# Kernel tuning notes

Hardware: AMD Instinct MI355X
Metric: run time of the kernel (lower is better)

Reference implementation:

```python
import jax, jax.numpy as jnp
import numpy as np

DT = 0.001
HIDDEN = 512
OUT = 128

def setup_inputs() -> dict:
    key = jax.random.key(0)
    k1, k2 = jax.random.split(key)
    x = jax.random.normal(k1, (64, 2048, HIDDEN), dtype=jnp.float32)
    # torch Linear default init ~ U(-1/sqrt(fan_in), 1/sqrt(fan_in)), weight shape [out, in]
    lim = 1.0 / np.sqrt(HIDDEN)
    W = jax.random.uniform(k2, (OUT, HIDDEN), dtype=jnp.float32, minval=-lim, maxval=lim)
    tau_syn = jnp.asarray(0.5, dtype=jnp.float32)  # tau_syn_out (used as tau_syn_inv)
    tau_mem = jnp.asarray(0.5, dtype=jnp.float32)  # tau_mem_out (used as tau_mem_inv)
    return {"x": x, "W": W, "tau_syn": tau_syn, "tau_mem": tau_mem}

def reference(x, W, tau_syn, tau_mem):
    # SNNDecode.forward: clamp taus, permute to [seq, batch, in], per-step
    # Linear + norse LI (leaky integrator) feed-forward step with v_leak = 0.
    tau_syn = jnp.clip(tau_syn, 0.0, 1.0)
    tau_mem = jnp.clip(tau_mem, 0.0, 1.0)
    batch, seq, _ = x.shape
    # The per-step Linear is recurrence-independent: hoist it into one big GEMM.
    # z_all: [seq, batch, out]
    z_all = jnp.einsum('bsh,oh->sbo', x, W)
    v0 = jnp.zeros((batch, OUT), dtype=x.dtype)
    i0 = jnp.zeros((batch, OUT), dtype=x.dtype)

    def step(carry, z):
        v, i = carry
        # li_feed_forward_step: dv = dt*tau_mem_inv*((v_leak - v) + i)
        v_new = v + DT * tau_mem * (i - v)
        i_dec = i - DT * tau_syn * i
        i_new = i_dec + z
        return (v_new, i_new), v_new

    (v_f, i_f), voltages = jax.lax.scan(step, (v0, i0), z_all)
    # output stacked over time: [seq, batch, out]; final state (v, i)
    return voltages, v_f, i_f
```

## Files before the change

### kernel.cpp

```cpp
#include <hip/hip_runtime.h>
#include <hip/hip_bf16.h>


typedef __attribute__((ext_vector_type(4))) float f4;
typedef __attribute__((ext_vector_type(8))) short s8;

#define SEQ    2048
#define HID    512
#define CHAINS 8192
#define VOLT   16777216
#define CHUNK  64
#define NCH    32

__device__ __forceinline__ float clamp01(float x) { return fminf(fmaxf(x, 0.f), 1.f); }

__device__ __forceinline__ short f2bf(float f) {
  union { float f; unsigned u; } c; c.f = f;
  unsigned u = c.u;
  unsigned r = (u + 0x7fffu + ((u >> 16) & 1u)) >> 16;
  return (short)r;
}

__device__ __forceinline__ int swz(int row, int k) {
  return (row * 64 + k) ^ ((row & 7) << 3);
}

__global__ __launch_bounds__(256) void k_wconv(const float* __restrict__ W,
                                               unsigned short* __restrict__ Wb) {
  const int i = blockIdx.x * 256 + threadIdx.x;
  const f4 lo = ((const f4*)W)[2 * i];
  const f4 hi = ((const f4*)W)[2 * i + 1];
  s8 v;
#pragma unroll
  for (int j = 0; j < 4; ++j) { v[j] = f2bf(lo[j]); v[j + 4] = f2bf(hi[j]); }
  ((s8*)Wb)[i] = v;
}

__global__ __launch_bounds__(256, 2) void k_gemm(const float* __restrict__ X,
                                                 const unsigned short* __restrict__ Wb,
                                                 float* __restrict__ Z) {
  __shared__ short As[2][128 * 64];
  __shared__ short Bs[2][128 * 64];
  const int tid = threadIdx.x;
  const int m0  = blockIdx.x << 7;
  const int b   = m0 >> 11;
  const int t0  = m0 & 2047;

  const int rbase = tid >> 3;
  const int coff  = (tid & 7) << 3;

  const int lane = tid & 63;
  const int wid  = tid >> 6;
  const int wmb  = (wid >> 1) << 6;
  const int wnb  = (wid & 1) << 6;
  const int lr   = lane & 15;
  const int lk   = (lane >> 4) << 3;

  const float* pX[4];
  const unsigned short* pW[4];
#pragma unroll
  for (int c = 0; c < 4; ++c) {
    const int row = (c << 5) + rbase;
    pX[c] = X + (size_t)(m0 + row) * HID + coff;
    pW[c] = Wb + (size_t)row * HID + coff;
  }

  f4 acc[4][4];
#pragma unroll
  for (int mi = 0; mi < 4; ++mi)
#pragma unroll
    for (int ni = 0; ni < 4; ++ni) acc[mi][ni] = (f4){0.f, 0.f, 0.f, 0.f};

  f4 xa[2][4][2];
  s8 wv[2][4];
#pragma unroll
  for (int c = 0; c < 4; ++c) {
    xa[0][c][0] = *(const f4*)(pX[c]);
    xa[0][c][1] = *(const f4*)(pX[c] + 4);
    wv[0][c]    = *(const s8*)(pW[c]);
  }

#pragma unroll
  for (int ks = 0; ks < 8; ++ks) {
    const int cur = ks & 1;
#pragma unroll
    for (int c = 0; c < 4; ++c) {
      const int row = (c << 5) + rbase;
      s8 va;
#pragma unroll
      for (int j = 0; j < 4; ++j) {
        va[j]     = f2bf(xa[cur][c][0][j]);
        va[j + 4] = f2bf(xa[cur][c][1][j]);
      }
      *(s8*)&As[cur][swz(row, coff)] = va;
      *(s8*)&Bs[cur][swz(row, coff)] = wv[cur][c];
    }
    if (ks < 7) {
      const int k0 = (ks + 1) << 6;
#pragma unroll
      for (int c = 0; c < 4; ++c) {
        xa[cur ^ 1][c][0] = *(const f4*)(pX[c] + k0);
        xa[cur ^ 1][c][1] = *(const f4*)(pX[c] + k0 + 4);
        wv[cur ^ 1][c]    = *(const s8*)(pW[c] + k0);
      }
    }
    __syncthreads();
#pragma unroll
    for (int kk = 0; kk < 2; ++kk) {
      s8 af[4], bg[4];
#pragma unroll
      for (int mi = 0; mi < 4; ++mi)
        af[mi] = *(const s8*)&As[cur][swz(wmb + (mi << 4) + lr, (kk << 5) + lk)];
#pragma unroll
      for (int ni = 0; ni < 4; ++ni)
        bg[ni] = *(const s8*)&Bs[cur][swz(wnb + (ni << 4) + lr, (kk << 5) + lk)];
#pragma unroll
      for (int mi = 0; mi < 4; ++mi)
#pragma unroll
        for (int ni = 0; ni < 4; ++ni)
          acc[mi][ni] = __builtin_amdgcn_mfma_f32_16x16x32_bf16(af[mi], bg[ni],
                                                                acc[mi][ni], 0, 0, 0);
    }
  }

  const int rr = (lane >> 4) << 2;
#pragma unroll
  for (int mi = 0; mi < 4; ++mi) {
    const int trow = t0 + wmb + (mi << 4) + rr;
#pragma unroll
    for (int ni = 0; ni < 4; ++ni) {
      const int col = wnb + (ni << 4) + lr;
#pragma unroll
      for (int r = 0; r < 4; ++r)
        Z[(size_t)(trow + r) * 8192 + (b << 7) + col] = acc[mi][ni][r];
    }
  }
}

__global__ __launch_bounds__(256) void k_states(const float* __restrict__ tau_syn,
                                                const float* __restrict__ tau_mem,
                                                const float* __restrict__ Z,
                                                float* __restrict__ ws) {
  const int tid = threadIdx.x;
  const int cg = (blockIdx.x & 31) * 64 + (tid & 63);
  const int q  = (blockIdx.x >> 5) * 4 + (tid >> 6);
  const float a  = 0.001f * clamp01(tau_mem[0]);
  const float bb = 0.001f * clamp01(tau_syn[0]);
  const float eb = 1.f - bb;
  const f4* z4 = (const f4*)Z;
  f4 v = (f4){0.f, 0.f, 0.f, 0.f}, ii = (f4){0.f, 0.f, 0.f, 0.f};
  const int tb = q << 6;
#pragma unroll 8
  for (int j = 0; j < CHUNK; ++j) {
    f4 z = z4[(size_t)(tb + j) * 2048 + cg];
    v  = v + a * (ii - v);
    ii = eb * ii + z;
  }
  f4* vend = (f4*)ws;
  f4* iend = vend + NCH * 2048;
  vend[q * 2048 + cg] = v;
  iend[q * 2048 + cg] = ii;
}

__global__ __launch_bounds__(256) void k_combine(const float* __restrict__ tau_syn,
                                                 const float* __restrict__ tau_mem,
                                                 float* __restrict__ Out,
                                                 float* __restrict__ ws) {
  const int c = blockIdx.x * 256 + threadIdx.x;
  const float a  = 0.001f * clamp01(tau_mem[0]);
  const float bb = 0.001f * clamp01(tau_syn[0]);
  const float ea = 1.f - a, eb = 1.f - bb;
  float P = 1.f, Q = 0.f, R = 1.f;
#pragma unroll
  for (int j = 0; j < CHUNK; ++j) { float Pn = P * ea; Q = P * a + Q * eb; P = Pn; R *= eb; }
  float* vend = ws;
  float* iend = ws + NCH * CHAINS;
  float sv = 0.f, si = 0.f;
  for (int q = 0; q < NCH; ++q) {
    const int idx = q * CHAINS + c;
    const float ve = vend[idx], ie = iend[idx];
    vend[idx] = sv;  iend[idx] = si;
    const float nv = P * sv + Q * si + ve;
    si = R * si + ie;
    sv = nv;
  }
  Out[VOLT + c] = sv;
  Out[VOLT + CHAINS + c] = si;
}

__global__ __launch_bounds__(256) void k_emit(const float* __restrict__ tau_syn,
                                              const float* __restrict__ tau_mem,
                                              float* Z,
                                              const float* __restrict__ ws) {
  const int tid = threadIdx.x;
  const int cg = (blockIdx.x & 31) * 64 + (tid & 63);
  const int q  = (blockIdx.x >> 5) * 4 + (tid >> 6);
  const float a  = 0.001f * clamp01(tau_mem[0]);
  const float bb = 0.001f * clamp01(tau_syn[0]);
  const float eb = 1.f - bb;
  f4* z4 = (f4*)Z;
  const f4* vin = (const f4*)ws;
  const f4* iin = vin + NCH * 2048;
  f4 v  = vin[q * 2048 + cg];
  f4 ii = iin[q * 2048 + cg];
  const int tb = q << 6;
#pragma unroll 8
  for (int j = 0; j < CHUNK; ++j) {
    const size_t idx = (size_t)(tb + j) * 2048 + cg;
    f4 z = z4[idx];
    v  = v + a * (ii - v);
    z4[idx] = v;
    ii = eb * ii + z;
  }
}

extern "C" void kernel_launch(void* const* d_in, const int* in_sizes, int n_in,
                              void* d_out, int out_size, void* d_ws, size_t ws_size,
                              hipStream_t stream) {
  const float* X   = (const float*)d_in[0];
  const float* W   = (const float*)d_in[1];
  const float* tsy = (const float*)d_in[2];
  const float* tme = (const float*)d_in[3];
  float* Out = (float*)d_out;
  float* ws  = (float*)d_ws;
  unsigned short* Wb = (unsigned short*)((char*)d_ws + (2u << 20));

  k_wconv<<<32, 256, 0, stream>>>(W, Wb);
  k_gemm<<<1024, 256, 0, stream>>>(X, Wb, Out);
  k_states<<<256, 256, 0, stream>>>(tsy, tme, Out, ws);
  k_combine<<<32, 256, 0, stream>>>(tsy, tme, Out, ws);
  k_emit<<<256, 256, 0, stream>>>(tsy, tme, Out, ws);
}
```

Measured before the change: 128.1 us.

## Fuse chunk-state scan into GEMM epilogue via shared-memory staged output

The separate k_states kernel is removed. Each GEMM block now stages its 128x128 output tile in shared memory, writes it to Z with coalesced float4 stores, and runs the per-chunk LI recurrence over its two 64-step halves straight from LDS, writing end states to the workspace. This saves one full read of Z from global memory and a kernel launch. The bf16 packing also switches to the packed __float22bfloat162_rn conversion, and the barrier moves so the next global prefetch is issued after the LDS write sync.

```diff
diff --git a/kernel.cpp b/kernel.cpp
--- a/kernel.cpp
+++ b/kernel.cpp
@@ -2,17 +2,24 @@
 #include <hip/hip_bf16.h>
 
 
-typedef __attribute__((ext_vector_type(4))) float f4;
-typedef __attribute__((ext_vector_type(8))) short s8;
+typedef __attribute__((ext_vector_type(4))) float    f4;
+typedef __attribute__((ext_vector_type(8))) short    s8;
+typedef __attribute__((ext_vector_type(4))) unsigned u4;
 
 #define SEQ    2048
 #define HID    512
 #define CHAINS 8192
 #define VOLT   16777216
-#define CHUNK  64
 #define NCH    32
 
 __device__ __forceinline__ float clamp01(float x) { return fminf(fmaxf(x, 0.f), 1.f); }
+
+__device__ __forceinline__ unsigned pkbf(float x, float y) {
+  float2 t; t.x = x; t.y = y;
+  union { __hip_bfloat162 h; unsigned u; } c;
+  c.h = __float22bfloat162_rn(t);
+  return c.u;
+}
 
 __device__ __forceinline__ short f2bf(float f) {
   union { float f; unsigned u; } c; c.f = f;
@@ -38,13 +45,20 @@
 
 __global__ __launch_bounds__(256, 2) void k_gemm(const float* __restrict__ X,
                                                  const unsigned short* __restrict__ Wb,
-                                                 float* __restrict__ Z) {
-  __shared__ short As[2][128 * 64];
-  __shared__ short Bs[2][128 * 64];
+                                                 float* __restrict__ Z,
+                                                 const float* __restrict__ tau_syn,
+                                                 const float* __restrict__ tau_mem,
+                                                 float* __restrict__ ws) {
+  __shared__ __align__(16) char smem[65536];
+  short* const AS = (short*)smem;
+  short* const BS = (short*)(smem + 32768);
+  float* const ZS = (float*)smem;
+
   const int tid = threadIdx.x;
-  const int m0  = blockIdx.x << 7;
-  const int b   = m0 >> 11;
-  const int t0  = m0 & 2047;
+  const int blk = blockIdx.x;
+  const int m0  = blk << 7;
+  const int bI  = blk >> 4;
+  const int t0  = (blk & 15) << 7;
 
   const int rbase = tid >> 3;
   const int coff  = (tid & 7) << 3;
@@ -83,18 +97,20 @@
 #pragma unroll
   for (int ks = 0; ks < 8; ++ks) {
     const int cur = ks & 1;
+    short* const Ac = AS + (cur << 13);
+    short* const Bc = BS + (cur << 13);
 #pragma unroll
     for (int c = 0; c < 4; ++c) {
       const int row = (c << 5) + rbase;
-      s8 va;
-#pragma unroll
-      for (int j = 0; j < 4; ++j) {
-        va[j]     = f2bf(xa[cur][c][0][j]);
-        va[j + 4] = f2bf(xa[cur][c][1][j]);
-      }
-      *(s8*)&As[cur][swz(row, coff)] = va;
-      *(s8*)&Bs[cur][swz(row, coff)] = wv[cur][c];
-    }
+      u4 va;
+      va[0] = pkbf(xa[cur][c][0][0], xa[cur][c][0][1]);
+      va[1] = pkbf(xa[cur][c][0][2], xa[cur][c][0][3]);
+      va[2] = pkbf(xa[cur][c][1][0], xa[cur][c][1][1]);
+      va[3] = pkbf(xa[cur][c][1][2], xa[cur][c][1][3]);
+      *(u4*)&Ac[swz(row, coff)] = va;
+      *(s8*)&Bc[swz(row, coff)] = wv[cur][c];
+    }
+    __syncthreads();
     if (ks < 7) {
       const int k0 = (ks + 1) << 6;
 #pragma unroll
@@ -104,16 +120,15 @@
         wv[cur ^ 1][c]    = *(const s8*)(pW[c] + k0);
       }
     }
-    __syncthreads();
 #pragma unroll
     for (int kk = 0; kk < 2; ++kk) {
       s8 af[4], bg[4];
 #pragma unroll
       for (int mi = 0; mi < 4; ++mi)
-        af[mi] = *(const s8*)&As[cur][swz(wmb + (mi << 4) + lr, (kk << 5) + lk)];
+        af[mi] = *(const s8*)&Ac[swz(wmb + (mi << 4) + lr, (kk << 5) + lk)];
 #pragma unroll
       for (int ni = 0; ni < 4; ++ni)
-        bg[ni] = *(const s8*)&Bs[cur][swz(wnb + (ni << 4) + lr, (kk << 5) + lk)];
+        bg[ni] = *(const s8*)&Bc[swz(wnb + (ni << 4) + lr, (kk << 5) + lk)];
 #pragma unroll
       for (int mi = 0; mi < 4; ++mi)
 #pragma unroll
@@ -123,43 +138,44 @@
     }
   }
 
+  __syncthreads();
   const int rr = (lane >> 4) << 2;
 #pragma unroll
-  for (int mi = 0; mi < 4; ++mi) {
-    const int trow = t0 + wmb + (mi << 4) + rr;
-#pragma unroll
-    for (int ni = 0; ni < 4; ++ni) {
-      const int col = wnb + (ni << 4) + lr;
+  for (int mi = 0; mi < 4; ++mi)
+#pragma unroll
+    for (int ni = 0; ni < 4; ++ni)
 #pragma unroll
       for (int r = 0; r < 4; ++r)
-        Z[(size_t)(trow + r) * 8192 + (b << 7) + col] = acc[mi][ni][r];
-    }
-  }
-}
-
-__global__ __launch_bounds__(256) void k_states(const float* __restrict__ tau_syn,
-                                                const float* __restrict__ tau_mem,
-                                                const float* __restrict__ Z,
-                                                float* __restrict__ ws) {
-  const int tid = threadIdx.x;
-  const int cg = (blockIdx.x & 31) * 64 + (tid & 63);
-  const int q  = (blockIdx.x >> 5) * 4 + (tid >> 6);
-  const float a  = 0.001f * clamp01(tau_mem[0]);
-  const float bb = 0.001f * clamp01(tau_syn[0]);
-  const float eb = 1.f - bb;
-  const f4* z4 = (const f4*)Z;
-  f4 v = (f4){0.f, 0.f, 0.f, 0.f}, ii = (f4){0.f, 0.f, 0.f, 0.f};
-  const int tb = q << 6;
+        ZS[(wmb + (mi << 4) + rr + r) * 128 + wnb + (ni << 4) + lr] = acc[mi][ni][r];
+  __syncthreads();
+
+  {
+    float* const Zrow = Z + (size_t)t0 * 8192 + (bI << 7);
+#pragma unroll
+    for (int i = 0; i < 16; ++i) {
+      const int idx  = (i << 8) + tid;
+      const int toff = idx >> 5;
+      const int c4   = idx & 31;
+      *(f4*)(Zrow + (size_t)toff * 8192 + (c4 << 2)) = *(const f4*)&ZS[toff * 128 + (c4 << 2)];
+    }
+  }
+  {
+    const float a  = 0.001f * clamp01(tau_mem[0]);
+    const float eb = 1.f - 0.001f * clamp01(tau_syn[0]);
+    const int h = tid >> 7, col = tid & 127;
+    const float* zs = ZS + ((h << 6) * 128) + col;
+    float v = 0.f, ii = 0.f;
 #pragma unroll 8
-  for (int j = 0; j < CHUNK; ++j) {
-    f4 z = z4[(size_t)(tb + j) * 2048 + cg];
-    v  = v + a * (ii - v);
-    ii = eb * ii + z;
-  }
-  f4* vend = (f4*)ws;
-  f4* iend = vend + NCH * 2048;
-  vend[q * 2048 + cg] = v;
-  iend[q * 2048 + cg] = ii;
+    for (int j = 0; j < 64; ++j) {
+      const float z = zs[j * 128];
+      v  = v + a * (ii - v);
+      ii = eb * ii + z;
+    }
+    const int q     = ((blk & 15) << 1) + h;
+    const int chain = (bI << 7) + col;
+    ws[q * CHAINS + chain]                 = v;
+    ws[NCH * CHAINS + q * CHAINS + chain]  = ii;
+  }
 }
 
 __global__ __launch_bounds__(256) void k_combine(const float* __restrict__ tau_syn,
@@ -172,7 +188,7 @@
   const float ea = 1.f - a, eb = 1.f - bb;
   float P = 1.f, Q = 0.f, R = 1.f;
 #pragma unroll
-  for (int j = 0; j < CHUNK; ++j) { float Pn = P * ea; Q = P * a + Q * eb; P = Pn; R *= eb; }
+  for (int j = 0; j < 64; ++j) { float Pn = P * ea; Q = P * a + Q * eb; P = Pn; R *= eb; }
   float* vend = ws;
   float* iend = ws + NCH * CHAINS;
   float sv = 0.f, si = 0.f;
@@ -196,8 +212,7 @@
   const int cg = (blockIdx.x & 31) * 64 + (tid & 63);
   const int q  = (blockIdx.x >> 5) * 4 + (tid >> 6);
   const float a  = 0.001f * clamp01(tau_mem[0]);
-  const float bb = 0.001f * clamp01(tau_syn[0]);
-  const float eb = 1.f - bb;
+  const float eb = 1.f - 0.001f * clamp01(tau_syn[0]);
   f4* z4 = (f4*)Z;
   const f4* vin = (const f4*)ws;
   const f4* iin = vin + NCH * 2048;
@@ -205,7 +220,7 @@
   f4 ii = iin[q * 2048 + cg];
   const int tb = q << 6;
 #pragma unroll 8
-  for (int j = 0; j < CHUNK; ++j) {
+  for (int j = 0; j < 64; ++j) {
     const size_t idx = (size_t)(tb + j) * 2048 + cg;
     f4 z = z4[idx];
     v  = v + a * (ii - v);
@@ -226,8 +241,7 @@
   unsigned short* Wb = (unsigned short*)((char*)d_ws + (2u << 20));
 
   k_wconv<<<32, 256, 0, stream>>>(W, Wb);
-  k_gemm<<<1024, 256, 0, stream>>>(X, Wb, Out);
-  k_states<<<256, 256, 0, stream>>>(tsy, tme, Out, ws);
+  k_gemm<<<1024, 256, 0, stream>>>(X, Wb, Out, tsy, tme, ws);
   k_combine<<<32, 256, 0, stream>>>(tsy, tme, Out, ws);
   k_emit<<<256, 256, 0, stream>>>(tsy, tme, Out, ws);
 }
```

Result: faster. 113.7 us (-11.3%).
